# Performance work log

Measured on AMD Instinct MI355X. Metric: run time of the kernel, lower is better.

Reference implementation:

```python
import jax, jax.numpy as jnp
import numpy as np

# ---- static module configuration (mirrors __init__) ----
BIG, SMALL = 13, 3
IN_C = 256
GHOST_RATIO = 0.23
NK = -(-BIG // SMALL)                          # ceil(13/3) = 5 small kernels tile the big one
REP_N = int(IN_C * (1 - GHOST_RATIO)) // 2 * 2 # 196 channels go through the big-kernel path
GHOST_N = IN_C - REP_N                         # 60 identity (ghost) channels
OUT_N = REP_N * NK                             # grouped conv channel-multiplier output
PAD = SMALL - 1                                # conv padding = 2 -> conv output is (H+2, W+2)
CROP = SMALL // 2                              # crop to emulate padding=k//2 on the small axis
MID = BIG // 2
REAL_PAD = [MID - i * SMALL - PAD for i in range(NK)]  # [4, 1, -2, -5, -8] shift offsets
P = BIG                                        # safe zero-pad for static shift slicing
N_PATH = 2
BN_EPS = 1e-5


def _split_indices():
    # exact replication of the module's fixed random ghost/rep channel split
    np.random.seed(123)
    ghost = np.sort(np.random.choice(IN_C, GHOST_N, replace=False))
    rep = np.sort(np.array(list(set(range(IN_C)) - set(ghost.tolist())), dtype=np.int64))
    return jnp.asarray(ghost, jnp.int32), jnp.asarray(rep, jnp.int32)


def _dwconv(x, w):
    # depthwise conv with channel multiplier NK: groups = REP_N
    return jax.lax.conv_general_dilated(
        x, w, window_strides=(1, 1), padding=[(PAD, PAD), (PAD, PAD)],
        dimension_numbers=('NCHW', 'OIHW', 'NCHW'), feature_group_count=REP_N)


def _bn(x, g, b):
    # BatchNorm2d in training mode (batch statistics), matching nn.(Sync)BatchNorm forward
    m = jnp.mean(x, axis=(0, 2, 3), keepdims=True)
    v = jnp.var(x, axis=(0, 2, 3), keepdims=True)
    return (x - m) * jax.lax.rsqrt(v + BN_EPS) * g[None, :, None, None] + b[None, :, None, None]


def setup_inputs() -> dict:
    key = jax.random.key(0)
    ks = jax.random.split(key, 4)
    B, H, W = 32, 56, 56
    inputs = jax.random.normal(ks[0], (B, IN_C, H, W), jnp.float32)
    fan = SMALL * SMALL  # groups=REP_N -> in_ch/groups = 1
    std = (2.0 / fan) ** 0.5
    w1 = jax.random.normal(ks[1], (OUT_N, 1, SMALL, SMALL), jnp.float32) * std
    w2 = jax.random.normal(ks[2], (OUT_N, 1, SMALL, SMALL), jnp.float32) * std
    ghost_idx, rep_idx = _split_indices()
    ones = jnp.ones((REP_N,), jnp.float32)
    zeros = jnp.zeros((REP_N,), jnp.float32)
    return {
        'inputs': inputs, 'w1': w1, 'w2': w2,
        'g1': ones, 'b1': zeros, 'g2': ones, 'b2': zeros, 'g3': ones, 'b3': zeros,
        'ghost_idx': ghost_idx, 'rep_idx': rep_idx,
    }


def reference(inputs, w1, w2, g1, b1, g2, b2, g3, b3, ghost_idx, rep_idx):
    B, C, H, W = inputs.shape
    rep_x = jnp.take(inputs, rep_idx, axis=1)      # [B, REP_N, H, W]
    ghost_x = jnp.take(inputs, ghost_idx, axis=1)  # [B, GHOST_N, H, W]

    # N_path grouped depthwise convs summed (pre-merge branch of the module)
    out = _dwconv(rep_x, w1) + _dwconv(rep_x, w2)  # [B, REP_N*NK, H+2, W+2]
    H2, W2 = out.shape[-2:]
    # grouped conv channel order: channel c -> outputs c*NK .. c*NK+NK-1
    x = out.reshape(B, REP_N, NK, H2, W2)

    # AddShift: stack the NK small-conv responses with shifts to emulate
    # a (BIG x SMALL) kernel (shift along H) and a (SMALL x BIG) kernel (shift along W).
    lora1 = jnp.zeros((B, REP_N, H, W), out.dtype)
    lora2 = jnp.zeros((B, REP_N, H, W), out.dtype)
    for i, r in enumerate(REAL_PAD):  # NK is a small static constant
        ci = x[:, :, i]  # [B, REP_N, H2, W2]
        yh = jnp.pad(ci, ((0, 0), (0, 0), (P, P), (0, 0)))
        lora1 = lora1 + yh[:, :, P - r:P - r + H, CROP:CROP + W]
        yw = jnp.pad(ci, ((0, 0), (0, 0), (0, 0), (P, P)))
        lora2 = lora2 + yw[:, :, CROP:CROP + H, P - r:P - r + W]
    # small-kernel branch: center chunk, cropped to emulate padding=SMALL//2
    small = x[:, :, NK // 2, CROP:CROP + H, CROP:CROP + W]

    y = _bn(lora1, g1, b1) + _bn(lora2, g2, b2) + _bn(small, g3, b3) + rep_x
    return jnp.concatenate([y, ghost_x], axis=1)  # [B, IN_C, H, W]
```

## Files before the change

kernel.cpp:

```cpp
#include <hip/hip_runtime.h>


#define B_    32
#define CIN   256
#define REPN  196
#define HW    56
#define IMG   3136
#define NTOT  (B_ * CIN * IMG)
#define NCONV1   2800
#define NCONV2R  1400
#define NGHOSTBLK 1920
#define STASH_ELEMS (B_ * REPN * IMG)

__device__ __forceinline__ void load_row20(float (&w)[20], const float* __restrict__ in,
                                           int base) {
  int i0 = base;      i0 = i0 < 0 ? 0 : i0;
  int i1 = base + 4;  i1 = i1 < 0 ? 0 : i1;
  int i3 = base + 12; i3 = i3 > (NTOT - 4) ? (NTOT - 4) : i3;
  int i4 = base + 16; i4 = i4 > (NTOT - 4) ? (NTOT - 4) : i4;
  const float4 v0 = *reinterpret_cast<const float4*>(in + i0);
  const float4 v1 = *reinterpret_cast<const float4*>(in + i1);
  const float4 v2 = *reinterpret_cast<const float4*>(in + base + 8);
  const float4 v3 = *reinterpret_cast<const float4*>(in + i3);
  const float4 v4 = *reinterpret_cast<const float4*>(in + i4);
  w[0]=v0.x;  w[1]=v0.y;  w[2]=v0.z;  w[3]=v0.w;
  w[4]=v1.x;  w[5]=v1.y;  w[6]=v1.z;  w[7]=v1.w;
  w[8]=v2.x;  w[9]=v2.y;  w[10]=v2.z; w[11]=v2.w;
  w[12]=v3.x; w[13]=v3.y; w[14]=v3.z; w[15]=v3.w;
  w[16]=v4.x; w[17]=v4.y; w[18]=v4.z; w[19]=v4.w;
}

__device__ __forceinline__ unsigned short pack_bf16(float f) {
  unsigned int u = __float_as_uint(f);
  u = u + 0x7FFFu + ((u >> 16) & 1u);
  return (unsigned short)(u >> 16);
}

#define ROW_COMPUTE(s_, wrow_, rm_)                                          \
  do {                                                                       \
    const int s = (s_);                                                      \
    const float f0 = ma * (rm_), f1 = mb * (rm_), f2 = (rm_),                \
                f3 = mc * (rm_), f4 = md * (rm_);                            \
    float win[20];                                                           \
    win[0]=wrow_[0]*f0;  win[1]=wrow_[1]*f0;  win[2]=wrow_[2]*f0;  win[3]=wrow_[3]*f0; \
    win[4]=wrow_[4]*f1;  win[5]=wrow_[5]*f1;  win[6]=wrow_[6]*f1;  win[7]=wrow_[7]*f1; \
    win[8]=wrow_[8]*f2;  win[9]=wrow_[9]*f2;  win[10]=wrow_[10]*f2; win[11]=wrow_[11]*f2; \
    win[12]=wrow_[12]*f3; win[13]=wrow_[13]*f3; win[14]=wrow_[14]*f3; win[15]=wrow_[15]*f3; \
    win[16]=wrow_[16]*f4; win[17]=wrow_[17]*f4; win[18]=wrow_[18]*f4; win[19]=wrow_[19]*f4; \
    _Pragma("unroll")                                                        \
    for (int lr = 0; lr < 8; ++lr) {                                         \
      const int t = s - lr;                                                  \
      if (t >= 0 && t < 15) {                                                \
        _Pragma("unroll")                                                    \
        for (int kw = 0; kw < 3; ++kw) {                                     \
          const float wgt = wv[3 * t + kw];                                  \
          _Pragma("unroll")                                                  \
          for (int dw = 0; dw < 4; ++dw)                                     \
            acc1[lr][dw] = fmaf(win[dw + kw + 7], wgt, acc1[lr][dw]);        \
        }                                                                    \
      }                                                                      \
    }                                                                        \
    _Pragma("unroll")                                                        \
    for (int lr = 0; lr < 8; ++lr) {                                         \
      const int kh = s - lr - 5;                                             \
      if (kh >= 0 && kh < 3) {                                               \
        _Pragma("unroll")                                                    \
        for (int T = 0; T < 15; ++T) {                                       \
          const float wgt = wv[(T / 3) * 9 + kh * 3 + (T % 3)];              \
          _Pragma("unroll")                                                  \
          for (int dw = 0; dw < 4; ++dw)                                     \
            acc2[lr % 3][dw] = fmaf(win[dw + T + 2], wgt, acc2[lr % 3][dw]); \
        }                                                                    \
        _Pragma("unroll")                                                    \
        for (int kw = 0; kw < 3; ++kw) {                                     \
          const float wgt = wv[18 + kh * 3 + kw];                            \
          _Pragma("unroll")                                                  \
          for (int dw = 0; dw < 4; ++dw)                                     \
            acc3[lr % 3][dw] = fmaf(win[dw + kw + 7], wgt, acc3[lr % 3][dw]); \
        }                                                                    \
      }                                                                      \
    }                                                                        \
    if (s >= 14) {                         \
      const int lr = s - 14;                                                 \
      _Pragma("unroll")                                                      \
      for (int dw = 0; dw < 4; ++dw) {                                       \
        const float v = acc1[lr][dw];                                        \
        s1 += v; q1 = fmaf(v, v, q1);                                        \
      }                                                                      \
      if (STASH) {                                                           \
        ushort4 t4;                                                          \
        t4.x = pack_bf16(acc1[lr][0]); t4.y = pack_bf16(acc1[lr][1]);        \
        t4.z = pack_bf16(acc1[lr][2]); t4.w = pack_bf16(acc1[lr][3]);        \
        *reinterpret_cast<ushort4*>(L1 + sbase + (h0 + lr) * HW + w0) = t4;  \
      }                                                                      \
    }                                                                        \
    if (s >= 7 && s <= 14) {         \
      const int lr = s - 7;                                                  \
      if (STASH) {                                                           \
        ushort4 t2, t3;                                                      \
        t2.x = pack_bf16(acc2[lr % 3][0]); t2.y = pack_bf16(acc2[lr % 3][1]); \
        t2.z = pack_bf16(acc2[lr % 3][2]); t2.w = pack_bf16(acc2[lr % 3][3]); \
        t3.x = pack_bf16(acc3[lr % 3][0]); t3.y = pack_bf16(acc3[lr % 3][1]); \
        t3.z = pack_bf16(acc3[lr % 3][2]); t3.w = pack_bf16(acc3[lr % 3][3]); \
        *reinterpret_cast<ushort4*>(L2 + sbase + (h0 + lr) * HW + w0) = t2;  \
        *reinterpret_cast<ushort4*>(S3 + sbase + (h0 + lr) * HW + w0) = t3;  \
      }                                                                      \
      _Pragma("unroll")                                                      \
      for (int dw = 0; dw < 4; ++dw) {                                       \
        const float v2 = acc2[lr % 3][dw], v3 = acc3[lr % 3][dw];            \
        s2 += v2; q2 = fmaf(v2, v2, q2);                                     \
        s3 += v3; q3 = fmaf(v3, v3, q3);                                     \
        acc2[lr % 3][dw] = 0.f;                                              \
        acc3[lr % 3][dw] = 0.f;                                              \
      }                                                                      \
    }                                                                        \
  } while (0)

template <bool STASH>
__launch_bounds__(256)
__global__ void sw_pass1(const float* __restrict__ in, const int* __restrict__ rep_idx,
                         const float* __restrict__ wsum, float* __restrict__ partial,
                         unsigned short* __restrict__ L1, unsigned short* __restrict__ L2,
                         unsigned short* __restrict__ S3) {
  const int bid = blockIdx.x;
  const int tid = threadIdx.x;

  const int c = (bid / 112) * 8 + (bid & 7);
  const int u = (bid % 112) >> 3;
  const int rb = u >> 1, bh = u & 1;
  if (c >= REPN) return;
  const int h0 = rb * 8;

  const int bloc = tid / 14;
  const int tw = tid - bloc * 14;
  const int w0 = tw * 4;
  const bool act = (bloc < 16);

  float wv[45];
  #pragma unroll
  for (int j = 0; j < 45; ++j) wv[j] = wsum[c * 45 + j];

  float s1 = 0, q1 = 0, s2 = 0, q2 = 0, s3 = 0, q3 = 0;

  if (act) {
    const int b = bh * 16 + bloc;
    const int src_c = rep_idx[c];
    const int ibase = (b * CIN + src_c) * IMG;
    const int sbase = (b * REPN + c) * IMG;

    const float ma = (tw >= 2) ? 1.f : 0.f;
    const float mb = (tw >= 1) ? 1.f : 0.f;
    const float mc = (tw <= 12) ? 1.f : 0.f;
    const float md = (tw <= 11) ? 1.f : 0.f;

    float acc1[8][4] = {};
    float acc2[3][4] = {};
    float acc3[3][4] = {};

    #pragma unroll
    for (int sp = 0; sp < 11; ++sp) {
      const int sA = 2 * sp, sB = 2 * sp + 1;
      const int rA0 = h0 - 6 + sA, rB0 = h0 - 6 + sB;
      const float rmA = (rA0 >= 0 && rA0 < HW) ? 1.f : 0.f;
      const float rmB = (rB0 >= 0 && rB0 < HW) ? 1.f : 0.f;
      const int rA = rA0 < 0 ? 0 : (rA0 > 55 ? 55 : rA0);
      const int rB = rB0 < 0 ? 0 : (rB0 > 55 ? 55 : rB0);
      float wA[20], wB[20];
      load_row20(wA, in, ibase + rA * HW + w0 - 8);
      load_row20(wB, in, ibase + rB * HW + w0 - 8);

      ROW_COMPUTE(sA, wA, rmA);
      ROW_COMPUTE(sB, wB, rmB);
    }
  }

  __shared__ float red[4][6];
  #pragma unroll
  for (int off = 32; off > 0; off >>= 1) {
    s1 += __shfl_down(s1, off); q1 += __shfl_down(q1, off);
    s2 += __shfl_down(s2, off); q2 += __shfl_down(q2, off);
    s3 += __shfl_down(s3, off); q3 += __shfl_down(q3, off);
  }
  const int lane = tid & 63, wid = tid >> 6;
  if (lane == 0) {
    red[wid][0] = s1; red[wid][1] = q1; red[wid][2] = s2;
    red[wid][3] = q2; red[wid][4] = s3; red[wid][5] = q3;
  }
  __syncthreads();
  if (tid < 6)
    partial[(c * 14 + u) * 6 + tid] =
        red[0][tid] + red[1][tid] + red[2][tid] + red[3][tid];
}

__launch_bounds__(448)
__global__ void sw_pass2r(const float* __restrict__ in, const int* __restrict__ rep_idx,
                          const int* __restrict__ ghost_idx, const float* __restrict__ wsum,
                          const float* __restrict__ stats2, float* __restrict__ out) {
  const int bid = blockIdx.x;
  const int tid = threadIdx.x;

  if (bid >= NCONV2R) {
    const int g = bid - NCONV2R;
    const int j = g >> 5, b = g & 31;
    const int src_c = ghost_idx[j];
    const float4* s = reinterpret_cast<const float4*>(in + (size_t)(b * CIN + src_c) * IMG);
    float4* d = reinterpret_cast<float4*>(out + ((size_t)(b * CIN) + REPN + j) * IMG);
    #pragma unroll 1
    for (int i = tid; i < 784; i += 448) d[i] = s[i];
    return;
  }

  const int c = (bid / 56) * 8 + (bid & 7);
  const int rb = (bid % 56) >> 3;
  if (c >= REPN) return;
  const int h0 = rb * 8;

  const int b = tid / 14;
  const int tw = tid - b * 14;
  const int w0 = tw * 4;
  const int src_c = rep_idx[c];
  const int ibase = (b * CIN + src_c) * IMG;

  float wv[45];
  #pragma unroll
  for (int j = 0; j < 45; ++j) wv[j] = wsum[c * 45 + j];

  const float A1 = stats2[c * 4 + 0], A2 = stats2[c * 4 + 1];
  const float A3 = stats2[c * 4 + 2], K_ = stats2[c * 4 + 3];

  const float ma = (tw >= 2) ? 1.f : 0.f;
  const float mb = (tw >= 1) ? 1.f : 0.f;
  const float mc = (tw <= 12) ? 1.f : 0.f;
  const float md = (tw <= 11) ? 1.f : 0.f;

  float acc1[8][4] = {};
  float acc2[3][4] = {};
  float acc3[3][4] = {};
  float stash[7][4];

  #pragma unroll
  for (int s = 0; s < 22; ++s) {
    const int r = h0 - 6 + s;
    if (r >= 0 && r < HW) {
      float win[20];
      load_row20(win, in, ibase + r * HW + w0 - 8);
      #pragma unroll
      for (int e = 0; e < 4; ++e) win[e] *= ma;
      #pragma unroll
      for (int e = 4; e < 8; ++e) win[e] *= mb;
      #pragma unroll
      for (int e = 12; e < 16; ++e) win[e] *= mc;
      #pragma unroll
      for (int e = 16; e < 20; ++e) win[e] *= md;

      #pragma unroll
      for (int lr = 0; lr < 8; ++lr) {
        const int t = s - lr;
        if (t >= 0 && t < 15) {
          #pragma unroll
          for (int kw = 0; kw < 3; ++kw) {
            const float wgt = wv[3 * t + kw];
            #pragma unroll
            for (int dw = 0; dw < 4; ++dw)
              acc1[lr][dw] = fmaf(win[dw + kw + 7], wgt, acc1[lr][dw]);
          }
        }
      }
      #pragma unroll
      for (int lr = 0; lr < 8; ++lr) {
        const int kh = s - lr - 5;
        if (kh >= 0 && kh < 3) {
          #pragma unroll
          for (int T = 0; T < 15; ++T) {
            const float wgt = wv[(T / 3) * 9 + kh * 3 + (T % 3)];
            #pragma unroll
            for (int dw = 0; dw < 4; ++dw)
              acc2[lr % 3][dw] = fmaf(win[dw + T + 2], wgt, acc2[lr % 3][dw]);
          }
          #pragma unroll
          for (int kw = 0; kw < 3; ++kw) {
            const float wgt = wv[18 + kh * 3 + kw];
            #pragma unroll
            for (int dw = 0; dw < 4; ++dw)
              acc3[lr % 3][dw] = fmaf(win[dw + kw + 7], wgt, acc3[lr % 3][dw]);
          }
        }
      }
    }

    if (s >= 14) {
      const int lr = s - 14;
      const int hh = h0 + lr;
      const float4 xv = *reinterpret_cast<const float4*>(in + ibase + hh * HW + w0);
      float4 o;
      o.x = fmaf(A1, acc1[lr][0], stash[lr % 7][0] + K_ + xv.x);
      o.y = fmaf(A1, acc1[lr][1], stash[lr % 7][1] + K_ + xv.y);
      o.z = fmaf(A1, acc1[lr][2], stash[lr % 7][2] + K_ + xv.z);
      o.w = fmaf(A1, acc1[lr][3], stash[lr % 7][3] + K_ + xv.w);
      *reinterpret_cast<float4*>(out + (size_t)(b * CIN + c) * IMG + hh * HW + w0) = o;
    }
    if (s >= 7 && s <= 14) {
      const int lr = s - 7;
      #pragma unroll
      for (int dw = 0; dw < 4; ++dw) {
        stash[lr % 7][dw] = fmaf(A2, acc2[lr % 3][dw], A3 * acc3[lr % 3][dw]);
        acc2[lr % 3][dw] = 0.f;
        acc3[lr % 3][dw] = 0.f;
      }
    }
  }
}

__launch_bounds__(256)
__global__ void sw_norm(const float* __restrict__ in, const int* __restrict__ rep_idx,
                        const int* __restrict__ ghost_idx, const float* __restrict__ stats2,
                        const unsigned short* __restrict__ L1,
                        const unsigned short* __restrict__ L2,
                        const unsigned short* __restrict__ S3,
                        float* __restrict__ out) {
  const int bid = blockIdx.x;
  const int tid = threadIdx.x;
  if (bid >= 6272) {
    const int g = bid - 6272;
    const int j = g >> 5, b = g & 31;
    const int src_c = ghost_idx[j];
    const float4* s = reinterpret_cast<const float4*>(in + (size_t)(b * CIN + src_c) * IMG);
    float4* d = reinterpret_cast<float4*>(out + ((size_t)(b * CIN) + REPN + j) * IMG);
    #pragma unroll 1
    for (int i = tid; i < 784; i += 256) d[i] = s[i];
    return;
  }
  const int c = bid >> 5, b = bid & 31;
  const float A1 = stats2[c * 4 + 0], A2 = stats2[c * 4 + 1];
  const float A3 = stats2[c * 4 + 2], K_ = stats2[c * 4 + 3];
  const int xb4 = (b * CIN + rep_idx[c]) * IMG / 4;
  const int ob4 = (b * CIN + c) * IMG / 4;
  const int sb4 = (b * REPN + c) * IMG / 4;
  const float4* xp = reinterpret_cast<const float4*>(in) + xb4;
  float4* op = reinterpret_cast<float4*>(out) + ob4;
  const ushort4* l1p = reinterpret_cast<const ushort4*>(L1) + sb4;
  const ushort4* l2p = reinterpret_cast<const ushort4*>(L2) + sb4;
  const ushort4* s3p = reinterpret_cast<const ushort4*>(S3) + sb4;
  #pragma unroll 1
  for (int g = tid; g < 784; g += 256) {
    const float4 x = xp[g];
    const ushort4 a = l1p[g], d2 = l2p[g], d3 = s3p[g];
    float4 y;
    y.x = fmaf(A1, __uint_as_float((unsigned)a.x << 16),
          fmaf(A2, __uint_as_float((unsigned)d2.x << 16),
          fmaf(A3, __uint_as_float((unsigned)d3.x << 16), K_ + x.x)));
    y.y = fmaf(A1, __uint_as_float((unsigned)a.y << 16),
          fmaf(A2, __uint_as_float((unsigned)d2.y << 16),
          fmaf(A3, __uint_as_float((unsigned)d3.y << 16), K_ + x.y)));
    y.z = fmaf(A1, __uint_as_float((unsigned)a.z << 16),
          fmaf(A2, __uint_as_float((unsigned)d2.z << 16),
          fmaf(A3, __uint_as_float((unsigned)d3.z << 16), K_ + x.z)));
    y.w = fmaf(A1, __uint_as_float((unsigned)a.w << 16),
          fmaf(A2, __uint_as_float((unsigned)d2.w << 16),
          fmaf(A3, __uint_as_float((unsigned)d3.w << 16), K_ + x.w)));
    op[g] = y;
  }
}

extern "C" __global__ void sw_prep(const float* __restrict__ w1, const float* __restrict__ w2,
                                   float* __restrict__ wsum) {
  int i = blockIdx.x * 256 + threadIdx.x;
  if (i < 8820) wsum[i] = w1[i] + w2[i];
}

extern "C" __global__ void sw_reduce(
    const float* __restrict__ partial,
    const float* __restrict__ g1, const float* __restrict__ b1,
    const float* __restrict__ g2, const float* __restrict__ b2,
    const float* __restrict__ g3, const float* __restrict__ b3,
    float* __restrict__ stats2) {
  const int c = blockIdx.x;
  const int tid = threadIdx.x;
  __shared__ float sm[6];
  if (tid < 6) {
    float s = 0;
    #pragma unroll
    for (int u = 0; u < 14; ++u) s += partial[(c * 14 + u) * 6 + tid];
    sm[tid] = s;
  }
  __syncthreads();
  if (tid == 0) {
    const float N = 100352.f;
    float m1 = sm[0] / N, v1 = sm[1] / N - m1 * m1;
    float m2 = sm[2] / N, v2 = sm[3] / N - m2 * m2;
    float m3 = sm[4] / N, v3 = sm[5] / N - m3 * m3;
    float A1 = g1[c] * rsqrtf(v1 + 1e-5f);
    float A2 = g2[c] * rsqrtf(v2 + 1e-5f);
    float A3 = g3[c] * rsqrtf(v3 + 1e-5f);
    float K = b1[c] + b2[c] + b3[c] - m1 * A1 - m2 * A2 - m3 * A3;
    stats2[c * 4 + 0] = A1; stats2[c * 4 + 1] = A2;
    stats2[c * 4 + 2] = A3; stats2[c * 4 + 3] = K;
  }
}

extern "C" void kernel_launch(void* const* d_in, const int* in_sizes, int n_in,
                              void* d_out, int out_size, void* d_ws, size_t ws_size,
                              hipStream_t stream) {
  const float* in  = (const float*)d_in[0];
  const float* w1  = (const float*)d_in[1];
  const float* w2  = (const float*)d_in[2];
  const float* g1  = (const float*)d_in[3];
  const float* b1  = (const float*)d_in[4];
  const float* g2  = (const float*)d_in[5];
  const float* b2  = (const float*)d_in[6];
  const float* g3  = (const float*)d_in[7];
  const float* b3  = (const float*)d_in[8];
  const int* ghost_idx = (const int*)d_in[9];
  const int* rep_idx   = (const int*)d_in[10];
  float* out = (float*)d_out;
  float* ws  = (float*)d_ws;

  float* wsum    = ws;
  float* stats2  = ws + 8832;
  float* partial = ws + 9728;
  unsigned short* L1 = reinterpret_cast<unsigned short*>((char*)d_ws + (1u << 18));
  unsigned short* L2 = L1 + STASH_ELEMS;
  unsigned short* S3 = L2 + STASH_ELEMS;
  const size_t need = (1u << 18) + 3ull * STASH_ELEMS * sizeof(unsigned short);

  sw_prep<<<35, 256, 0, stream>>>(w1, w2, wsum);
  if (ws_size >= need) {
    sw_pass1<true><<<NCONV1, 256, 0, stream>>>(in, rep_idx, wsum, partial, L1, L2, S3);
    sw_reduce<<<196, 64, 0, stream>>>(partial, g1, b1, g2, b2, g3, b3, stats2);
    sw_norm<<<6272 + NGHOSTBLK, 256, 0, stream>>>(in, rep_idx, ghost_idx, stats2,
                                                  L1, L2, S3, out);
  } else {
    sw_pass1<false><<<NCONV1, 256, 0, stream>>>(in, rep_idx, wsum, partial, L1, L2, S3);
    sw_reduce<<<196, 64, 0, stream>>>(partial, g1, b1, g2, b2, g3, b3, stats2);
    sw_pass2r<<<NCONV2R + NGHOSTBLK, 448, 0, stream>>>(in, rep_idx, ghost_idx, wsum,
                                                       stats2, out);
  }
}
```

Measured before the change: 178.9 us.

## Use 448-thread blocks covering all batches, prefetch rows, and skip out-of-range rows

Pass 1 now launches 1400 blocks of 448 threads, so each block covers all 32 batch images for one channel and row band instead of splitting them into two halves. The old 256-thread layout left some threads idle. Input rows are software-pipelined: the next row's five float4 loads are issued before the current row is computed, to hide global load latency. Rows that fall entirely outside the image at the first and last bands are skipped instead of being multiplied by a zero mask. The deeper prefetch and wider block raise register pressure and may reduce occupancy, and the partial-sum layout changes from 14 to 7 slices per channel.

```diff
diff --git a/kernel.cpp b/kernel.cpp
--- a/kernel.cpp
+++ b/kernel.cpp
@@ -7,7 +7,7 @@
 #define HW    56
 #define IMG   3136
 #define NTOT  (B_ * CIN * IMG)
-#define NCONV1   2800
+#define NCONV1   1400
 #define NCONV2R  1400
 #define NGHOSTBLK 1920
 #define STASH_ELEMS (B_ * REPN * IMG)
@@ -36,47 +36,63 @@
   return (unsigned short)(u >> 16);
 }
 
-#define ROW_COMPUTE(s_, wrow_, rm_)                                          \
+#define RBASE(s_) (ibase + (((h0 - 6 + (s_)) < 0) ? 0 : (((h0 - 6 + (s_)) > 55) ? 55 : (h0 - 6 + (s_)))) * HW + wo8)
+
+#define ISSUE5(P0,P1,P2,P3,P4, base_)                                        \
+  do {                                                                       \
+    const int bse = (base_);                                                 \
+    int i0 = bse;      i0 = i0 < 0 ? 0 : i0;                                 \
+    int i1 = bse + 4;  i1 = i1 < 0 ? 0 : i1;                                 \
+    int i3 = bse + 12; i3 = i3 > (NTOT - 4) ? (NTOT - 4) : i3;               \
+    int i4 = bse + 16; i4 = i4 > (NTOT - 4) ? (NTOT - 4) : i4;               \
+    P0 = *reinterpret_cast<const float4*>(in + i0);                          \
+    P1 = *reinterpret_cast<const float4*>(in + i1);                          \
+    P2 = *reinterpret_cast<const float4*>(in + bse + 8);                     \
+    P3 = *reinterpret_cast<const float4*>(in + i3);                          \
+    P4 = *reinterpret_cast<const float4*>(in + i4);                          \
+  } while (0)
+
+#define STEP(s_, P0,P1,P2,P3,P4)                                             \
   do {                                                                       \
     const int s = (s_);                                                      \
-    const float f0 = ma * (rm_), f1 = mb * (rm_), f2 = (rm_),                \
-                f3 = mc * (rm_), f4 = md * (rm_);                            \
-    float win[20];                                                           \
-    win[0]=wrow_[0]*f0;  win[1]=wrow_[1]*f0;  win[2]=wrow_[2]*f0;  win[3]=wrow_[3]*f0; \
-    win[4]=wrow_[4]*f1;  win[5]=wrow_[5]*f1;  win[6]=wrow_[6]*f1;  win[7]=wrow_[7]*f1; \
-    win[8]=wrow_[8]*f2;  win[9]=wrow_[9]*f2;  win[10]=wrow_[10]*f2; win[11]=wrow_[11]*f2; \
-    win[12]=wrow_[12]*f3; win[13]=wrow_[13]*f3; win[14]=wrow_[14]*f3; win[15]=wrow_[15]*f3; \
-    win[16]=wrow_[16]*f4; win[17]=wrow_[17]*f4; win[18]=wrow_[18]*f4; win[19]=wrow_[19]*f4; \
-    _Pragma("unroll")                                                        \
-    for (int lr = 0; lr < 8; ++lr) {                                         \
-      const int t = s - lr;                                                  \
-      if (t >= 0 && t < 15) {                                                \
-        _Pragma("unroll")                                                    \
-        for (int kw = 0; kw < 3; ++kw) {                                     \
-          const float wgt = wv[3 * t + kw];                                  \
+    if (s >= s_lo && s <= s_hi) {                                            \
+      float win[20];                                                         \
+      win[0]=P0.x*ma;  win[1]=P0.y*ma;  win[2]=P0.z*ma;  win[3]=P0.w*ma;     \
+      win[4]=P1.x*mb;  win[5]=P1.y*mb;  win[6]=P1.z*mb;  win[7]=P1.w*mb;     \
+      win[8]=P2.x;     win[9]=P2.y;     win[10]=P2.z;    win[11]=P2.w;       \
+      win[12]=P3.x*mc; win[13]=P3.y*mc; win[14]=P3.z*mc; win[15]=P3.w*mc;    \
+      win[16]=P4.x*md; win[17]=P4.y*md; win[18]=P4.z*md; win[19]=P4.w*md;    \
+      _Pragma("unroll")                                                      \
+      for (int lr = 0; lr < 8; ++lr) {                                       \
+        const int t = s - lr;                                                \
+        if (t >= 0 && t < 15) {                                              \
           _Pragma("unroll")                                                  \
-          for (int dw = 0; dw < 4; ++dw)                                     \
-            acc1[lr][dw] = fmaf(win[dw + kw + 7], wgt, acc1[lr][dw]);        \
+          for (int kw = 0; kw < 3; ++kw) {                                   \
+            const float wgt = wv[3 * t + kw];                                \
+            _Pragma("unroll")                                                \
+            for (int dw = 0; dw < 4; ++dw)                                   \
+              acc1[lr][dw] = fmaf(win[dw + kw + 7], wgt, acc1[lr][dw]);      \
+          }                                                                  \
         }                                                                    \
       }                                                                      \
-    }                                                                        \
-    _Pragma("unroll")                                                        \
-    for (int lr = 0; lr < 8; ++lr) {                                         \
-      const int kh = s - lr - 5;                                             \
-      if (kh >= 0 && kh < 3) {                                               \
-        _Pragma("unroll")                                                    \
-        for (int T = 0; T < 15; ++T) {                                       \
-          const float wgt = wv[(T / 3) * 9 + kh * 3 + (T % 3)];              \
+      _Pragma("unroll")                                                      \
+      for (int lr = 0; lr < 8; ++lr) {                                       \
+        const int kh = s - lr - 5;                                           \
+        if (kh >= 0 && kh < 3) {                                             \
           _Pragma("unroll")                                                  \
-          for (int dw = 0; dw < 4; ++dw)                                     \
-            acc2[lr % 3][dw] = fmaf(win[dw + T + 2], wgt, acc2[lr % 3][dw]); \
-        }                                                                    \
-        _Pragma("unroll")                                                    \
-        for (int kw = 0; kw < 3; ++kw) {                                     \
-          const float wgt = wv[18 + kh * 3 + kw];                            \
+          for (int T = 0; T < 15; ++T) {                                     \
+            const float wgt = wv[(T / 3) * 9 + kh * 3 + (T % 3)];            \
+            _Pragma("unroll")                                                \
+            for (int dw = 0; dw < 4; ++dw)                                   \
+              acc2[lr % 3][dw] = fmaf(win[dw + T + 2], wgt, acc2[lr % 3][dw]); \
+          }                                                                  \
           _Pragma("unroll")                                                  \
-          for (int dw = 0; dw < 4; ++dw)                                     \
-            acc3[lr % 3][dw] = fmaf(win[dw + kw + 7], wgt, acc3[lr % 3][dw]); \
+          for (int kw = 0; kw < 3; ++kw) {                                   \
+            const float wgt = wv[18 + kh * 3 + kw];                          \
+            _Pragma("unroll")                                                \
+            for (int dw = 0; dw < 4; ++dw)                                   \
+              acc3[lr % 3][dw] = fmaf(win[dw + kw + 7], wgt, acc3[lr % 3][dw]); \
+          }                                                                  \
         }                                                                    \
       }                                                                      \
     }                                                                        \
@@ -84,8 +100,8 @@
       const int lr = s - 14;                                                 \
       _Pragma("unroll")                                                      \
       for (int dw = 0; dw < 4; ++dw) {                                       \
-        const float v = acc1[lr][dw];                                        \
-        s1 += v; q1 = fmaf(v, v, q1);                                        \
+        const float x = acc1[lr][dw];                                        \
+        s1 += x; q1 = fmaf(x, x, q1);                                        \
       }                                                                      \
       if (STASH) {                                                           \
         ushort4 t4;                                                          \
@@ -117,7 +133,7 @@
   } while (0)
 
 template <bool STASH>
-__launch_bounds__(256)
+__launch_bounds__(448)
 __global__ void sw_pass1(const float* __restrict__ in, const int* __restrict__ rep_idx,
                          const float* __restrict__ wsum, float* __restrict__ partial,
                          unsigned short* __restrict__ L1, unsigned short* __restrict__ L2,
@@ -125,56 +141,52 @@
   const int bid = blockIdx.x;
   const int tid = threadIdx.x;
 
-  const int c = (bid / 112) * 8 + (bid & 7);
-  const int u = (bid % 112) >> 3;
-  const int rb = u >> 1, bh = u & 1;
+  const int c = (bid / 56) * 8 + (bid & 7);
+  const int rb = (bid % 56) >> 3;
   if (c >= REPN) return;
   const int h0 = rb * 8;
 
-  const int bloc = tid / 14;
-  const int tw = tid - bloc * 14;
+  const int b = tid / 14;
+  const int tw = tid - b * 14;
   const int w0 = tw * 4;
-  const bool act = (bloc < 16);
+  const int src_c = rep_idx[c];
+  const int ibase = (b * CIN + src_c) * IMG;
+  const int sbase = (b * REPN + c) * IMG;
+  const int wo8 = w0 - 8;
 
   float wv[45];
   #pragma unroll
   for (int j = 0; j < 45; ++j) wv[j] = wsum[c * 45 + j];
 
+  const float ma = (tw >= 2) ? 1.f : 0.f;
+  const float mb = (tw >= 1) ? 1.f : 0.f;
+  const float mc = (tw <= 12) ? 1.f : 0.f;
+  const float md = (tw <= 11) ? 1.f : 0.f;
+
+  const int s_lo = (rb == 0) ? 6 : 0;
+  const int s_hi = (rb == 6) ? 13 : 21;
+
+  float acc1[8][4] = {};
+  float acc2[3][4] = {};
+  float acc3[3][4] = {};
   float s1 = 0, q1 = 0, s2 = 0, q2 = 0, s3 = 0, q3 = 0;
 
-  if (act) {
-    const int b = bh * 16 + bloc;
-    const int src_c = rep_idx[c];
-    const int ibase = (b * CIN + src_c) * IMG;
-    const int sbase = (b * REPN + c) * IMG;
-
-    const float ma = (tw >= 2) ? 1.f : 0.f;
-    const float mb = (tw >= 1) ? 1.f : 0.f;
-    const float mc = (tw <= 12) ? 1.f : 0.f;
-    const float md = (tw <= 11) ? 1.f : 0.f;
-
-    float acc1[8][4] = {};
-    float acc2[3][4] = {};
-    float acc3[3][4] = {};
-
-    #pragma unroll
-    for (int sp = 0; sp < 11; ++sp) {
-      const int sA = 2 * sp, sB = 2 * sp + 1;
-      const int rA0 = h0 - 6 + sA, rB0 = h0 - 6 + sB;
-      const float rmA = (rA0 >= 0 && rA0 < HW) ? 1.f : 0.f;
-      const float rmB = (rB0 >= 0 && rB0 < HW) ? 1.f : 0.f;
-      const int rA = rA0 < 0 ? 0 : (rA0 > 55 ? 55 : rA0);
-      const int rB = rB0 < 0 ? 0 : (rB0 > 55 ? 55 : rB0);
-      float wA[20], wB[20];
-      load_row20(wA, in, ibase + rA * HW + w0 - 8);
-      load_row20(wB, in, ibase + rB * HW + w0 - 8);
-
-      ROW_COMPUTE(sA, wA, rmA);
-      ROW_COMPUTE(sB, wB, rmB);
-    }
-  }
-
-  __shared__ float red[4][6];
+  float4 pA0, pA1, pA2, pA3, pA4;
+  float4 pB0, pB1, pB2, pB3, pB4;
+
+  ISSUE5(pA0, pA1, pA2, pA3, pA4, RBASE(0));
+
+  #pragma unroll
+  for (int sp = 0; sp < 11; ++sp) {
+    const int sE = 2 * sp, sO = 2 * sp + 1;
+    ISSUE5(pB0, pB1, pB2, pB3, pB4, RBASE(sO));
+    STEP(sE, pA0, pA1, pA2, pA3, pA4);
+    if (sp < 10)
+      ISSUE5(pA0, pA1, pA2, pA3, pA4, RBASE(sO + 1));
+    STEP(sO, pB0, pB1, pB2, pB3, pB4);
+  }
+
+  __shared__ float red[7][6];
   #pragma unroll
   for (int off = 32; off > 0; off >>= 1) {
     s1 += __shfl_down(s1, off); q1 += __shfl_down(q1, off);
@@ -187,9 +199,12 @@
     red[wid][3] = q2; red[wid][4] = s3; red[wid][5] = q3;
   }
   __syncthreads();
-  if (tid < 6)
-    partial[(c * 14 + u) * 6 + tid] =
-        red[0][tid] + red[1][tid] + red[2][tid] + red[3][tid];
+  if (tid < 6) {
+    float t = 0;
+    #pragma unroll
+    for (int w = 0; w < 7; ++w) t += red[w][tid];
+    partial[(c * 7 + rb) * 6 + tid] = t;
+  }
 }
 
 __launch_bounds__(448)
@@ -380,7 +395,7 @@
   if (tid < 6) {
     float s = 0;
     #pragma unroll
-    for (int u = 0; u < 14; ++u) s += partial[(c * 14 + u) * 6 + tid];
+    for (int rb = 0; rb < 7; ++rb) s += partial[(c * 7 + rb) * 6 + tid];
     sm[tid] = s;
   }
   __syncthreads();
@@ -425,12 +440,12 @@
 
   sw_prep<<<35, 256, 0, stream>>>(w1, w2, wsum);
   if (ws_size >= need) {
-    sw_pass1<true><<<NCONV1, 256, 0, stream>>>(in, rep_idx, wsum, partial, L1, L2, S3);
+    sw_pass1<true><<<NCONV1, 448, 0, stream>>>(in, rep_idx, wsum, partial, L1, L2, S3);
     sw_reduce<<<196, 64, 0, stream>>>(partial, g1, b1, g2, b2, g3, b3, stats2);
     sw_norm<<<6272 + NGHOSTBLK, 256, 0, stream>>>(in, rep_idx, ghost_idx, stats2,
                                                   L1, L2, S3, out);
   } else {
-    sw_pass1<false><<<NCONV1, 256, 0, stream>>>(in, rep_idx, wsum, partial, L1, L2, S3);
+    sw_pass1<false><<<NCONV1, 448, 0, stream>>>(in, rep_idx, wsum, partial, L1, L2, S3);
     sw_reduce<<<196, 64, 0, stream>>>(partial, g1, b1, g2, b2, g3, b3, stats2);
     sw_pass2r<<<NCONV2R + NGHOSTBLK, 448, 0, stream>>>(in, rep_idx, ghost_idx, wsum,
                                                        stats2, out);
```

After: 251.6 us. +40.7%, slower.
